# Kernel tuning notes

Hardware: AMD Instinct MI355X
Metric: run time of the kernel (lower is better)

Reference implementation:

```python
import jax, jax.numpy as jnp
import numpy as np

DIFF_Q = 0.8
ONE_OVER_DIFF_TOT = 0.05234482976098482

# roll shifts reproducing the 26 neighbor slices in make_pairs (periodic wrap).
# torch slice [2:] of the wrap-padded tensor == neighbor at +1 == jnp.roll(q, -1, axis)
SHIFTS = [
    (-1, 0, 0), (1, 0, 0), (0, -1, 0), (0, 1, 0), (0, 0, -1), (0, 0, 1),
    (-1, -1, 0), (1, -1, 0), (-1, 1, 0), (1, 1, 0),
    (-1, 0, -1), (1, 0, -1), (-1, 0, 1), (1, 0, 1),
    (0, -1, -1), (0, 1, -1), (0, -1, 1), (0, 1, 1),
    (-1, -1, -1), (-1, -1, 1), (-1, 1, -1), (-1, 1, 1),
    (1, -1, -1), (1, -1, 1), (1, 1, -1), (1, 1, 1),
]
# 6 face neighbors (d=1), 12 edge neighbors (d=sqrt2), 8 corner neighbors (d=sqrt3)
D_INV = jnp.asarray(np.array([1.0] * 6 + [2 ** -0.5] * 12 + [3 ** -0.5] * 8, dtype=np.float32))


def _mlp(x, params):
    # tanh-activated MLP, linear final layer (matches nn.Sequential built in __init__)
    for W, b in params[:-1]:
        x = jnp.tanh(x @ W.T + b)
    W, b = params[-1]
    return x @ W.T + b


def setup_inputs() -> dict:
    key = jax.random.key(0)
    ks = jax.random.split(key, 11)
    q = jax.random.uniform(ks[0], (1, 48, 48, 48, 2), dtype=jnp.float32)
    def lin(k, fan_out, fan_in):
        k1, k2 = jax.random.split(k)
        bound = 1.0 / np.sqrt(fan_in)
        W = jax.random.uniform(k1, (fan_out, fan_in), jnp.float32, -bound, bound)
        b = jax.random.uniform(k2, (fan_out,), jnp.float32, -bound, bound)
        return W, b
    W0, b0 = lin(ks[1], 16, 4)
    W1, b1 = lin(ks[2], 16, 16)
    W2, b2 = lin(ks[3], 16, 16)
    W3, b3 = lin(ks[4], 16, 16)
    Wout, bout = lin(ks[5], 1, 16)
    return {"q": q, "W0": W0, "b0": b0, "W1": W1, "b1": b1, "W2": W2, "b2": b2,
            "W3": W3, "b3": b3, "Wout": Wout, "bout": bout}


def reference(q, W0, b0, W1, b1, W2, b2, W3, b3, Wout, bout):
    # make_pairs detaches q, and q_updated starts from q.detach().clone()
    qd = jax.lax.stop_gradient(q)
    # neighbors: [B,X,Y,Z,26,2]
    nb = jnp.stack([jnp.roll(qd, s, axis=(1, 2, 3)) for s in SHIFTS], axis=4)
    own = jnp.broadcast_to(qd[:, :, :, :, None, :], nb.shape)
    x1 = jnp.concatenate([own, nb], axis=-1)  # [B,X,Y,Z,26,4]
    x2 = jnp.concatenate([nb, own], axis=-1)  # channel-rolled version
    params = [(W0, b0), (W1, b1), (W2, b2), (W3, b3), (Wout, bout)]
    transfer = jnp.tanh(_mlp(x1, params) - _mlp(x2, params))[..., 0]  # [B,X,Y,Z,26]
    # negative transfer scaled by own charge, positive by neighbor charge
    factor = jnp.where(transfer < 0, own[..., 0], nb[..., 0])
    transfer = (transfer * factor * D_INV).sum(axis=4) * (ONE_OVER_DIFF_TOT * DIFF_Q)
    return qd.at[..., 0].add(transfer)
```

## Files before the change

kernel.cpp:

```cpp
#include <hip/hip_runtime.h>

static constexpr int NSIDE = 48;
static constexpr int NVOX  = NSIDE * NSIDE * NSIDE;
static constexpr float SCALE = 0.041875863808787856f;
static constexpr int NDIR  = 13;
static constexpr int PAIRS_PER_BLOCK = 128;
static constexpr int BLOCKS_PER_DIR  = NVOX / PAIRS_PER_BLOCK;

typedef _Float16 f16x8 __attribute__((ext_vector_type(8)));
typedef float    f32x16 __attribute__((ext_vector_type(16)));

__device__ __constant__ int g_ox[NDIR] = { 1, 0, 0,  1, 1, 1, 1, 0, 0,  1, 1, 1, 1 };
__device__ __constant__ int g_oy[NDIR] = { 0, 1, 0,  1,-1, 0, 0, 1, 1,  1, 1,-1,-1 };
__device__ __constant__ int g_oz[NDIR] = { 0, 0, 1,  0, 0, 1,-1, 1,-1,  1,-1, 1,-1 };
__device__ __constant__ float g_dinv[NDIR] = {
    1.f, 1.f, 1.f,
    0.70710678118654752f, 0.70710678118654752f, 0.70710678118654752f,
    0.70710678118654752f, 0.70710678118654752f, 0.70710678118654752f,
    0.57735026918962576f, 0.57735026918962576f, 0.57735026918962576f, 0.57735026918962576f };

__device__ __constant__ int c_ox[26] = { 1,-1, 0, 0, 0, 0,
                                         1,-1, 1,-1, 1,-1, 1,-1, 0, 0, 0, 0,
                                         1, 1, 1, 1,-1,-1,-1,-1 };
__device__ __constant__ int c_oy[26] = { 0, 0, 1,-1, 0, 0,
                                         1, 1,-1,-1, 0, 0, 0, 0, 1,-1, 1,-1,
                                         1, 1,-1,-1, 1, 1,-1,-1 };
__device__ __constant__ int c_oz[26] = { 0, 0, 0, 0, 1,-1,
                                         0, 0, 0, 0, 1, 1,-1,-1, 1, 1,-1,-1,
                                         1,-1, 1,-1, 1,-1, 1,-1 };
__device__ __constant__ float c_dinv[26] = {
    1.f, 1.f, 1.f, 1.f, 1.f, 1.f,
    0.70710678118654752f, 0.70710678118654752f, 0.70710678118654752f, 0.70710678118654752f,
    0.70710678118654752f, 0.70710678118654752f, 0.70710678118654752f, 0.70710678118654752f,
    0.70710678118654752f, 0.70710678118654752f, 0.70710678118654752f, 0.70710678118654752f,
    0.57735026918962576f, 0.57735026918962576f, 0.57735026918962576f, 0.57735026918962576f,
    0.57735026918962576f, 0.57735026918962576f, 0.57735026918962576f, 0.57735026918962576f };

__device__ __forceinline__ float fast_tanh(float x) {
    float e = __builtin_amdgcn_exp2f(x * 2.8853900817779268f);
    float r = __builtin_amdgcn_rcpf(e + 1.0f);
    return fmaf(-2.0f, r, 1.0f);
}

#define STAGE_WEIGHTS()                                                        \
    __shared__ __align__(16) float sw[916];                                    \
    {                                                                          \
        const int t_ = threadIdx.x;                                            \
        if (t_ <  64) sw[      t_] = W0[t_];                                   \
        if (t_ <  16) sw[ 64 + t_] = b0[t_];                                   \
                      sw[ 80 + t_] = W1[t_];                                   \
        if (t_ <  16) sw[336 + t_] = b1[t_];                                   \
                      sw[352 + t_] = W2[t_];                                   \
        if (t_ <  16) sw[608 + t_] = b2[t_];                                   \
                      sw[624 + t_] = W3[t_];                                   \
        if (t_ <  16) sw[880 + t_] = b3[t_];                                   \
        if (t_ <  16) sw[896 + t_] = Wout[t_];                                 \
        if (t_ ==  0) sw[912]     = bout[0];                                   \
        __syncthreads();                                                       \
    }

#define SIG(G, P) (((P) < 4) ? 4 * (G) + (P) : 8 + 4 * (G) + ((P) - 4))

__global__ __launch_bounds__(256)
void flux_mfma_kernel(const float* __restrict__ q,
                      const float* __restrict__ W0, const float* __restrict__ b0,
                      const float* __restrict__ W1, const float* __restrict__ b1,
                      const float* __restrict__ W2, const float* __restrict__ b2,
                      const float* __restrict__ W3, const float* __restrict__ b3,
                      const float* __restrict__ Wout, const float* __restrict__ bout,
                      float* __restrict__ ws)
{
    STAGE_WEIGHTS()

    const int k    = blockIdx.x / BLOCKS_PER_DIR;
    const int rem  = blockIdx.x - k * BLOCKS_PER_DIR;
    const int lane = threadIdx.x & 63;
    const int wv   = threadIdx.x >> 6;
    const int g    = lane >> 5;
    const int vox  = rem * PAIRS_PER_BLOCK + wv * 32 + (lane & 31);

    const int z = vox % NSIDE;
    const int y = (vox / NSIDE) % NSIDE;
    const int x = vox / (NSIDE * NSIDE);
    const int ox = g_ox[k], oy = g_oy[k], oz = g_oz[k];
    const int nx = (ox > 0) ? ((x == NSIDE - 1) ? 0 : x + 1) : x;
    const int ny = (oy > 0) ? ((y == NSIDE - 1) ? 0 : y + 1)
                            : ((oy < 0) ? ((y == 0) ? NSIDE - 1 : y - 1) : y);
    const int nz = (oz > 0) ? ((z == NSIDE - 1) ? 0 : z + 1)
                            : ((oz < 0) ? ((z == 0) ? NSIDE - 1 : z - 1) : z);

    const float2 own = reinterpret_cast<const float2*>(q)[vox];
    const float2 nbq = reinterpret_cast<const float2*>(q)[(nx * NSIDE + ny) * NSIDE + nz];
    const float o0 = own.x, o1 = own.y;
    const float n0 = nbq.x, n1 = nbq.y;

    const int row = lane & 31;
    const int wr  = (row & 15) * 16;
    f16x8 aw1, aw2, aw3;
    f32x16 c1, c2, c3;
    #pragma unroll
    for (int p = 0; p < 8; ++p) {
        const int kk = SIG(g, p);
        aw1[p] = (_Float16)sw[ 80 + wr + kk];
        aw2[p] = (_Float16)sw[352 + wr + kk];
        aw3[p] = (_Float16)sw[624 + wr + kk];
        c1[p] = sw[336 + kk];
        c2[p] = sw[608 + kk];
        c3[p] = sw[880 + kk];
    }
    #pragma unroll
    for (int p = 8; p < 16; ++p) { c1[p] = 0.0f; c2[p] = 0.0f; c3[p] = 0.0f; }
    float woutv[8];
    #pragma unroll
    for (int p = 0; p < 8; ++p) woutv[p] = sw[896 + SIG(g, p)];

    f16x8 ba, bb;
    #pragma unroll
    for (int p = 0; p < 8; ++p) {
        const int f = SIG(g, p);
        const float4 w = *reinterpret_cast<const float4*>(&sw[f * 4]);
        const float bbias = sw[64 + f];
        float pa = fmaf(w.x, o0, fmaf(w.y, o1, fmaf(w.z, n0, fmaf(w.w, n1, bbias))));
        float pb = fmaf(w.x, n0, fmaf(w.y, n1, fmaf(w.z, o0, fmaf(w.w, o1, bbias))));
        ba[p] = (_Float16)fast_tanh(pa);
        bb[p] = (_Float16)fast_tanh(pb);
    }

    f32x16 da, db;
    da = __builtin_amdgcn_mfma_f32_32x32x16_f16(aw1, ba, c1, 0, 0, 0);
    db = __builtin_amdgcn_mfma_f32_32x32x16_f16(aw1, bb, c1, 0, 0, 0);
    #pragma unroll
    for (int p = 0; p < 8; ++p) {
        ba[p] = (_Float16)fast_tanh(da[p]);
        bb[p] = (_Float16)fast_tanh(db[p]);
    }
    da = __builtin_amdgcn_mfma_f32_32x32x16_f16(aw2, ba, c2, 0, 0, 0);
    db = __builtin_amdgcn_mfma_f32_32x32x16_f16(aw2, bb, c2, 0, 0, 0);
    #pragma unroll
    for (int p = 0; p < 8; ++p) {
        ba[p] = (_Float16)fast_tanh(da[p]);
        bb[p] = (_Float16)fast_tanh(db[p]);
    }
    da = __builtin_amdgcn_mfma_f32_32x32x16_f16(aw3, ba, c3, 0, 0, 0);
    db = __builtin_amdgcn_mfma_f32_32x32x16_f16(aw3, bb, c3, 0, 0, 0);

    float pa = 0.0f, pb = 0.0f;
    #pragma unroll
    for (int p = 0; p < 8; ++p) {
        pa = fmaf(fast_tanh(da[p]), woutv[p], pa);
        pb = fmaf(fast_tanh(db[p]), woutv[p], pb);
    }
    pa += __shfl_xor(pa, 32);
    pb += __shfl_xor(pb, 32);

    const float tr  = fast_tanh(pa - pb);
    const float fac = (tr < 0.0f) ? o0 : n0;
    if ((lane & 63) < 32)
        ws[k * NVOX + vox] = tr * fac * g_dinv[k];
}

__global__ __launch_bounds__(256)
void gather_kernel(const float* __restrict__ q,
                   const float* __restrict__ ws,
                   float* __restrict__ out)
{
    const int vox = blockIdx.x * 256 + threadIdx.x;

    const int z = vox % NSIDE;
    const int y = (vox / NSIDE) % NSIDE;
    const int x = vox / (NSIDE * NSIDE);
    const int xm = (x == 0) ? NSIDE - 1 : x - 1;
    const int ym = (y == 0) ? NSIDE - 1 : y - 1;
    const int yp = (y == NSIDE - 1) ? 0 : y + 1;
    const int zm = (z == 0) ? NSIDE - 1 : z - 1;
    const int zp = (z == NSIDE - 1) ? 0 : z + 1;

    float s = 0.0f;
    #pragma unroll
    for (int k = 0; k < NDIR; ++k) {
        const int px = g_ox[k] ? xm : x;
        const int py = (g_oy[k] > 0) ? ym : ((g_oy[k] < 0) ? yp : y);
        const int pz = (g_oz[k] > 0) ? zm : ((g_oz[k] < 0) ? zp : z);
        s += ws[k * NVOX + vox];
        s -= ws[k * NVOX + (px * NSIDE + py) * NSIDE + pz];
    }

    const float2 own = reinterpret_cast<const float2*>(q)[vox];
    float2 r;
    r.x = fmaf(s, SCALE, own.x);
    r.y = own.y;
    reinterpret_cast<float2*>(out)[vox] = r;
}

#define LAYER(WB, INA, INB, OUTA, OUTB)                                        \
    {                                                                          \
        _Pragma("unroll")                                                      \
        for (int i = 0; i < 16; ++i) {                                         \
            float aa = sw[(WB) + 256 + i];                                     \
            float ab = aa;                                                     \
            _Pragma("unroll")                                                  \
            for (int kk = 0; kk < 4; ++kk) {                                   \
                const float4 w = *reinterpret_cast<const float4*>(             \
                    &sw[(WB) + i * 16 + kk * 4]);                              \
                aa = fmaf(w.x, INA[4 * kk + 0], aa);                           \
                aa = fmaf(w.y, INA[4 * kk + 1], aa);                           \
                aa = fmaf(w.z, INA[4 * kk + 2], aa);                           \
                aa = fmaf(w.w, INA[4 * kk + 3], aa);                           \
                ab = fmaf(w.x, INB[4 * kk + 0], ab);                           \
                ab = fmaf(w.y, INB[4 * kk + 1], ab);                           \
                ab = fmaf(w.z, INB[4 * kk + 2], ab);                           \
                ab = fmaf(w.w, INB[4 * kk + 3], ab);                           \
            }                                                                  \
            OUTA[i] = fast_tanh(aa);                                           \
            OUTB[i] = fast_tanh(ab);                                           \
        }                                                                      \
    }

__global__ __launch_bounds__(256)
void automaton_kernel(const float* __restrict__ q,
                      const float* __restrict__ W0, const float* __restrict__ b0,
                      const float* __restrict__ W1, const float* __restrict__ b1,
                      const float* __restrict__ W2, const float* __restrict__ b2,
                      const float* __restrict__ W3, const float* __restrict__ b3,
                      const float* __restrict__ Wout, const float* __restrict__ bout,
                      float* __restrict__ out)
{
    STAGE_WEIGHTS()

    const int gid  = blockIdx.x * 256 + threadIdx.x;
    const int vox  = gid >> 1;
    const int half = gid & 1;

    const int z = vox % NSIDE;
    const int y = (vox / NSIDE) % NSIDE;
    const int x = vox / (NSIDE * NSIDE);
    const int xm = (x == 0) ? NSIDE - 1 : x - 1;
    const int xp = (x == NSIDE - 1) ? 0 : x + 1;
    const int ym = (y == 0) ? NSIDE - 1 : y - 1;
    const int yp = (y == NSIDE - 1) ? 0 : y + 1;
    const int zm = (z == 0) ? NSIDE - 1 : z - 1;
    const int zp = (z == NSIDE - 1) ? 0 : z + 1;

    const float2 own = reinterpret_cast<const float2*>(q)[vox];
    const float o0 = own.x, o1 = own.y;

    float sum = 0.0f;
    #pragma unroll 1
    for (int k = half * 13; k < half * 13 + 13; ++k) {
        asm volatile("" ::: "memory");
        const int ox = c_ox[k], oy = c_oy[k], oz = c_oz[k];
        const int nx = (ox < 0) ? xm : ((ox > 0) ? xp : x);
        const int ny = (oy < 0) ? ym : ((oy > 0) ? yp : y);
        const int nz = (oz < 0) ? zm : ((oz > 0) ? zp : z);
        const float2 nbq = reinterpret_cast<const float2*>(q)[(nx * NSIDE + ny) * NSIDE + nz];
        const float n0 = nbq.x, n1 = nbq.y;

        float ha[16], hb[16], ta[16], tb[16];
        #pragma unroll
        for (int i = 0; i < 16; ++i) {
            const float4 w = *reinterpret_cast<const float4*>(&sw[i * 4]);
            const float bbias = sw[64 + i];
            float pa = fmaf(w.x, o0, fmaf(w.y, o1, fmaf(w.z, n0, fmaf(w.w, n1, bbias))));
            float pb = fmaf(w.x, n0, fmaf(w.y, n1, fmaf(w.z, o0, fmaf(w.w, o1, bbias))));
            ha[i] = fast_tanh(pa);
            hb[i] = fast_tanh(pb);
        }
        LAYER(80,  ha, hb, ta, tb)
        LAYER(352, ta, tb, ha, hb)
        LAYER(624, ha, hb, ta, tb)
        float oa = sw[912], ob = sw[912];
        #pragma unroll
        for (int kk = 0; kk < 4; ++kk) {
            const float4 w = *reinterpret_cast<const float4*>(&sw[896 + kk * 4]);
            oa = fmaf(w.x, ta[4 * kk + 0], oa);
            oa = fmaf(w.y, ta[4 * kk + 1], oa);
            oa = fmaf(w.z, ta[4 * kk + 2], oa);
            oa = fmaf(w.w, ta[4 * kk + 3], oa);
            ob = fmaf(w.x, tb[4 * kk + 0], ob);
            ob = fmaf(w.y, tb[4 * kk + 1], ob);
            ob = fmaf(w.z, tb[4 * kk + 2], ob);
            ob = fmaf(w.w, tb[4 * kk + 3], ob);
        }
        const float tr  = fast_tanh(oa - ob);
        const float fac = (tr < 0.0f) ? o0 : n0;
        sum = fmaf(tr * fac, c_dinv[k], sum);
    }

    sum += __shfl_xor(sum, 1);
    if (half == 0) {
        float2 r;
        r.x = fmaf(sum, SCALE, o0);
        r.y = o1;
        reinterpret_cast<float2*>(out)[vox] = r;
    }
}

extern "C" void kernel_launch(void* const* d_in, const int* in_sizes, int n_in,
                              void* d_out, int out_size, void* d_ws, size_t ws_size,
                              hipStream_t stream) {
    const float* q    = (const float*)d_in[0];
    const float* W0   = (const float*)d_in[1];
    const float* b0   = (const float*)d_in[2];
    const float* W1   = (const float*)d_in[3];
    const float* b1   = (const float*)d_in[4];
    const float* W2   = (const float*)d_in[5];
    const float* b2   = (const float*)d_in[6];
    const float* W3   = (const float*)d_in[7];
    const float* b3   = (const float*)d_in[8];
    const float* Wout = (const float*)d_in[9];
    const float* bout = (const float*)d_in[10];
    float* out = (float*)d_out;

    const size_t ws_needed = (size_t)NDIR * NVOX * sizeof(float);
    if (ws_size >= ws_needed) {
        float* ws = (float*)d_ws;
        flux_mfma_kernel<<<dim3(NDIR * BLOCKS_PER_DIR), dim3(256), 0, stream>>>(
            q, W0, b0, W1, b1, W2, b2, W3, b3, Wout, bout, ws);
        gather_kernel<<<dim3(NVOX / 256), dim3(256), 0, stream>>>(q, ws, out);
    } else {
        automaton_kernel<<<dim3(NVOX * 2 / 256), dim3(256), 0, stream>>>(
            q, W0, b0, W1, b1, W2, b2, W3, b3, Wout, bout, out);
    }
}
```

Measured before the change: 63.80 us.

## Move first MLP layer onto MFMA and replace tanh with shared-reciprocal Pade

The first layer (4->16) now runs as an MFMA with zero-padded weights and inputs, instead of per-lane scalar FMAs. The hidden-layer tanh switches from exp2+rcp to a clamped [7/6] Pade rational approximation that shares one reciprocal between the two branch evaluations. This cuts transcendental instructions and scalar FMA work, at the cost of two extra MFMAs and reduced tanh accuracy for large inputs. The clamp keeps outputs in [-1,1], but the approximation error near saturation may matter for correctness tolerance.

```diff
diff --git a/kernel.cpp b/kernel.cpp
--- a/kernel.cpp
+++ b/kernel.cpp
@@ -42,6 +42,19 @@
     return fmaf(-2.0f, r, 1.0f);
 }
 
+__device__ __forceinline__ void pade_tanh_duo(float xa, float xb, float& ta, float& tb) {
+    const float ua = xa * xa, ub = xb * xb;
+    const float na = fmaf(ua, ua + 105.0f, 945.0f);
+    const float nb = fmaf(ub, ub + 105.0f, 945.0f);
+    const float ea = fmaf(ua, fmaf(ua, 15.0f, 420.0f), 945.0f);
+    const float eb = fmaf(ub, fmaf(ub, 15.0f, 420.0f), 945.0f);
+    const float R  = __builtin_amdgcn_rcpf(ea * eb);
+    ta = (xa * na) * (eb * R);
+    tb = (xb * nb) * (ea * R);
+    ta = fminf(1.0f, fmaxf(-1.0f, ta));
+    tb = fminf(1.0f, fmaxf(-1.0f, tb));
+}
+
 #define STAGE_WEIGHTS()                                                        \
     __shared__ __align__(16) float sw[916];                                    \
     {                                                                          \
@@ -95,51 +108,68 @@
     const float n0 = nbq.x, n1 = nbq.y;
 
     const int row = lane & 31;
-    const int wr  = (row & 15) * 16;
-    f16x8 aw1, aw2, aw3;
-    f32x16 c1, c2, c3;
+    f16x8 aw0, aw1, aw2, aw3;
+    f32x16 c0, c1, c2, c3;
     #pragma unroll
     for (int p = 0; p < 8; ++p) {
         const int kk = SIG(g, p);
-        aw1[p] = (_Float16)sw[ 80 + wr + kk];
-        aw2[p] = (_Float16)sw[352 + wr + kk];
-        aw3[p] = (_Float16)sw[624 + wr + kk];
+        aw0[p] = (row < 16 && kk < 4) ? (_Float16)sw[row * 4 + kk] : (_Float16)0.0f;
+        const float w1v = (row < 16) ? sw[ 80 + (row & 15) * 16 + kk] : 0.0f;
+        const float w2v = (row < 16) ? sw[352 + (row & 15) * 16 + kk] : 0.0f;
+        const float w3v = (row < 16) ? sw[624 + (row & 15) * 16 + kk] : 0.0f;
+        aw1[p] = (_Float16)w1v;
+        aw2[p] = (_Float16)w2v;
+        aw3[p] = (_Float16)w3v;
+        c0[p] = sw[ 64 + kk];
         c1[p] = sw[336 + kk];
         c2[p] = sw[608 + kk];
         c3[p] = sw[880 + kk];
     }
     #pragma unroll
-    for (int p = 8; p < 16; ++p) { c1[p] = 0.0f; c2[p] = 0.0f; c3[p] = 0.0f; }
+    for (int p = 8; p < 16; ++p) { c0[p] = 0.0f; c1[p] = 0.0f; c2[p] = 0.0f; c3[p] = 0.0f; }
     float woutv[8];
     #pragma unroll
     for (int p = 0; p < 8; ++p) woutv[p] = sw[896 + SIG(g, p)];
 
     f16x8 ba, bb;
-    #pragma unroll
-    for (int p = 0; p < 8; ++p) {
-        const int f = SIG(g, p);
-        const float4 w = *reinterpret_cast<const float4*>(&sw[f * 4]);
-        const float bbias = sw[64 + f];
-        float pa = fmaf(w.x, o0, fmaf(w.y, o1, fmaf(w.z, n0, fmaf(w.w, n1, bbias))));
-        float pb = fmaf(w.x, n0, fmaf(w.y, n1, fmaf(w.z, o0, fmaf(w.w, o1, bbias))));
-        ba[p] = (_Float16)fast_tanh(pa);
-        bb[p] = (_Float16)fast_tanh(pb);
+    {
+        const float va[4] = { o0, o1, n0, n1 };
+        #pragma unroll
+        for (int p = 0; p < 8; ++p) {
+            const float fa = (g == 0 && p < 4) ? va[p & 3]       : 0.0f;
+            const float fb = (g == 0 && p < 4) ? va[(p & 3) ^ 2] : 0.0f;
+            ba[p] = (_Float16)fa;
+            bb[p] = (_Float16)fb;
+        }
     }
 
     f32x16 da, db;
+    da = __builtin_amdgcn_mfma_f32_32x32x16_f16(aw0, ba, c0, 0, 0, 0);
+    db = __builtin_amdgcn_mfma_f32_32x32x16_f16(aw0, bb, c0, 0, 0, 0);
+    #pragma unroll
+    for (int p = 0; p < 8; ++p) {
+        float ta, tb;
+        pade_tanh_duo(da[p], db[p], ta, tb);
+        ba[p] = (_Float16)ta;
+        bb[p] = (_Float16)tb;
+    }
     da = __builtin_amdgcn_mfma_f32_32x32x16_f16(aw1, ba, c1, 0, 0, 0);
     db = __builtin_amdgcn_mfma_f32_32x32x16_f16(aw1, bb, c1, 0, 0, 0);
     #pragma unroll
     for (int p = 0; p < 8; ++p) {
-        ba[p] = (_Float16)fast_tanh(da[p]);
-        bb[p] = (_Float16)fast_tanh(db[p]);
+        float ta, tb;
+        pade_tanh_duo(da[p], db[p], ta, tb);
+        ba[p] = (_Float16)ta;
+        bb[p] = (_Float16)tb;
     }
     da = __builtin_amdgcn_mfma_f32_32x32x16_f16(aw2, ba, c2, 0, 0, 0);
     db = __builtin_amdgcn_mfma_f32_32x32x16_f16(aw2, bb, c2, 0, 0, 0);
     #pragma unroll
     for (int p = 0; p < 8; ++p) {
-        ba[p] = (_Float16)fast_tanh(da[p]);
-        bb[p] = (_Float16)fast_tanh(db[p]);
+        float ta, tb;
+        pade_tanh_duo(da[p], db[p], ta, tb);
+        ba[p] = (_Float16)ta;
+        bb[p] = (_Float16)tb;
     }
     da = __builtin_amdgcn_mfma_f32_32x32x16_f16(aw3, ba, c3, 0, 0, 0);
     db = __builtin_amdgcn_mfma_f32_32x32x16_f16(aw3, bb, c3, 0, 0, 0);
@@ -147,15 +177,17 @@
     float pa = 0.0f, pb = 0.0f;
     #pragma unroll
     for (int p = 0; p < 8; ++p) {
-        pa = fmaf(fast_tanh(da[p]), woutv[p], pa);
-        pb = fmaf(fast_tanh(db[p]), woutv[p], pb);
+        float ta, tb;
+        pade_tanh_duo(da[p], db[p], ta, tb);
+        pa = fmaf(ta, woutv[p], pa);
+        pb = fmaf(tb, woutv[p], pb);
     }
     pa += __shfl_xor(pa, 32);
     pb += __shfl_xor(pb, 32);
 
     const float tr  = fast_tanh(pa - pb);
     const float fac = (tr < 0.0f) ? o0 : n0;
-    if ((lane & 63) < 32)
+    if (lane < 32)
         ws[k * NVOX + vox] = tr * fac * g_dinv[k];
 }
 
```

After: 83.35 us. +30.6%, slower.

## Loop over several directions per flux block to amortize weight staging

Applied to the files above, without the earlier changes.

The flux kernel now launches one block per group of voxels and a slice, with each block iterating over 3-4 neighbor directions instead of handling a single direction. Weight staging into shared memory, MFMA weight-fragment setup, own-charge load and wrap index computation are done once per block and reused across directions. This reduces redundant setup work and block launch overhead, at the cost of fewer blocks and serial per-block work that may reduce latency hiding.

```diff
diff --git a/kernel.cpp b/kernel.cpp
--- a/kernel.cpp
+++ b/kernel.cpp
@@ -4,8 +4,9 @@
 static constexpr int NVOX  = NSIDE * NSIDE * NSIDE;
 static constexpr float SCALE = 0.041875863808787856f;
 static constexpr int NDIR  = 13;
-static constexpr int PAIRS_PER_BLOCK = 128;
-static constexpr int BLOCKS_PER_DIR  = NVOX / PAIRS_PER_BLOCK;
+static constexpr int NVOXGRP = NVOX / 32;
+static constexpr int NSLICE  = 4;
+static constexpr int FLUX_BLOCKS = NVOXGRP;
 
 typedef _Float16 f16x8 __attribute__((ext_vector_type(8)));
 typedef float    f32x16 __attribute__((ext_vector_type(16)));
@@ -42,7 +43,7 @@
     return fmaf(-2.0f, r, 1.0f);
 }
 
-#define STAGE_WEIGHTS()                                                        \
+#define STAGE_WEIGHTS_256()                                                    \
     __shared__ __align__(16) float sw[916];                                    \
     {                                                                          \
         const int t_ = threadIdx.x;                                            \
@@ -70,32 +71,28 @@
                       const float* __restrict__ Wout, const float* __restrict__ bout,
                       float* __restrict__ ws)
 {
-    STAGE_WEIGHTS()
-
-    const int k    = blockIdx.x / BLOCKS_PER_DIR;
-    const int rem  = blockIdx.x - k * BLOCKS_PER_DIR;
-    const int lane = threadIdx.x & 63;
-    const int wv   = threadIdx.x >> 6;
-    const int g    = lane >> 5;
-    const int vox  = rem * PAIRS_PER_BLOCK + wv * 32 + (lane & 31);
+    STAGE_WEIGHTS_256()
+
+    const int lane  = threadIdx.x & 63;
+    const int wv    = threadIdx.x >> 6;
+    const int g     = lane >> 5;
+    const int slice = blockIdx.x / (FLUX_BLOCKS / NSLICE);
+    const int vgrp  = (blockIdx.x % (FLUX_BLOCKS / NSLICE)) * 4 + wv;
+    const int vox   = vgrp * 32 + (lane & 31);
 
     const int z = vox % NSIDE;
     const int y = (vox / NSIDE) % NSIDE;
     const int x = vox / (NSIDE * NSIDE);
-    const int ox = g_ox[k], oy = g_oy[k], oz = g_oz[k];
-    const int nx = (ox > 0) ? ((x == NSIDE - 1) ? 0 : x + 1) : x;
-    const int ny = (oy > 0) ? ((y == NSIDE - 1) ? 0 : y + 1)
-                            : ((oy < 0) ? ((y == 0) ? NSIDE - 1 : y - 1) : y);
-    const int nz = (oz > 0) ? ((z == NSIDE - 1) ? 0 : z + 1)
-                            : ((oz < 0) ? ((z == 0) ? NSIDE - 1 : z - 1) : z);
+    const int xp = (x == NSIDE - 1) ? 0 : x + 1;
+    const int ym = (y == 0) ? NSIDE - 1 : y - 1;
+    const int yp = (y == NSIDE - 1) ? 0 : y + 1;
+    const int zm = (z == 0) ? NSIDE - 1 : z - 1;
+    const int zp = (z == NSIDE - 1) ? 0 : z + 1;
 
     const float2 own = reinterpret_cast<const float2*>(q)[vox];
-    const float2 nbq = reinterpret_cast<const float2*>(q)[(nx * NSIDE + ny) * NSIDE + nz];
     const float o0 = own.x, o1 = own.y;
-    const float n0 = nbq.x, n1 = nbq.y;
-
-    const int row = lane & 31;
-    const int wr  = (row & 15) * 16;
+
+    const int wr = (lane & 15) * 16;
     f16x8 aw1, aw2, aw3;
     f32x16 c1, c2, c3;
     #pragma unroll
@@ -114,49 +111,64 @@
     #pragma unroll
     for (int p = 0; p < 8; ++p) woutv[p] = sw[896 + SIG(g, p)];
 
-    f16x8 ba, bb;
-    #pragma unroll
-    for (int p = 0; p < 8; ++p) {
-        const int f = SIG(g, p);
-        const float4 w = *reinterpret_cast<const float4*>(&sw[f * 4]);
-        const float bbias = sw[64 + f];
-        float pa = fmaf(w.x, o0, fmaf(w.y, o1, fmaf(w.z, n0, fmaf(w.w, n1, bbias))));
-        float pb = fmaf(w.x, n0, fmaf(w.y, n1, fmaf(w.z, o0, fmaf(w.w, o1, bbias))));
-        ba[p] = (_Float16)fast_tanh(pa);
-        bb[p] = (_Float16)fast_tanh(pb);
-    }
-
-    f32x16 da, db;
-    da = __builtin_amdgcn_mfma_f32_32x32x16_f16(aw1, ba, c1, 0, 0, 0);
-    db = __builtin_amdgcn_mfma_f32_32x32x16_f16(aw1, bb, c1, 0, 0, 0);
-    #pragma unroll
-    for (int p = 0; p < 8; ++p) {
-        ba[p] = (_Float16)fast_tanh(da[p]);
-        bb[p] = (_Float16)fast_tanh(db[p]);
-    }
-    da = __builtin_amdgcn_mfma_f32_32x32x16_f16(aw2, ba, c2, 0, 0, 0);
-    db = __builtin_amdgcn_mfma_f32_32x32x16_f16(aw2, bb, c2, 0, 0, 0);
-    #pragma unroll
-    for (int p = 0; p < 8; ++p) {
-        ba[p] = (_Float16)fast_tanh(da[p]);
-        bb[p] = (_Float16)fast_tanh(db[p]);
-    }
-    da = __builtin_amdgcn_mfma_f32_32x32x16_f16(aw3, ba, c3, 0, 0, 0);
-    db = __builtin_amdgcn_mfma_f32_32x32x16_f16(aw3, bb, c3, 0, 0, 0);
-
-    float pa = 0.0f, pb = 0.0f;
-    #pragma unroll
-    for (int p = 0; p < 8; ++p) {
-        pa = fmaf(fast_tanh(da[p]), woutv[p], pa);
-        pb = fmaf(fast_tanh(db[p]), woutv[p], pb);
-    }
-    pa += __shfl_xor(pa, 32);
-    pb += __shfl_xor(pb, 32);
-
-    const float tr  = fast_tanh(pa - pb);
-    const float fac = (tr < 0.0f) ? o0 : n0;
-    if ((lane & 63) < 32)
-        ws[k * NVOX + vox] = tr * fac * g_dinv[k];
+    const int kb = (slice == 0) ? 0 : (slice == 1) ? 4 : (slice == 2) ? 7 : 10;
+    const int ke = (slice == 0) ? 4 : (slice == 1) ? 7 : (slice == 2) ? 10 : 13;
+
+    #pragma unroll 1
+    for (int k = kb; k < ke; ++k) {
+        asm volatile("" ::: "memory");
+
+        const int ox = g_ox[k], oy = g_oy[k], oz = g_oz[k];
+        const int nx = ox ? xp : x;
+        const int ny = (oy > 0) ? yp : ((oy < 0) ? ym : y);
+        const int nz = (oz > 0) ? zp : ((oz < 0) ? zm : z);
+        const float2 nbq = reinterpret_cast<const float2*>(q)[(nx * NSIDE + ny) * NSIDE + nz];
+        const float n0 = nbq.x, n1 = nbq.y;
+
+        f16x8 ba, bb;
+        #pragma unroll
+        for (int p = 0; p < 8; ++p) {
+            const int f = SIG(g, p);
+            const float4 w = *reinterpret_cast<const float4*>(&sw[f * 4]);
+            const float bbias = sw[64 + f];
+            float pa = fmaf(w.x, o0, fmaf(w.y, o1, fmaf(w.z, n0, fmaf(w.w, n1, bbias))));
+            float pb = fmaf(w.x, n0, fmaf(w.y, n1, fmaf(w.z, o0, fmaf(w.w, o1, bbias))));
+            ba[p] = (_Float16)fast_tanh(pa);
+            bb[p] = (_Float16)fast_tanh(pb);
+        }
+
+        f32x16 da, db;
+        da = __builtin_amdgcn_mfma_f32_32x32x16_f16(aw1, ba, c1, 0, 0, 0);
+        db = __builtin_amdgcn_mfma_f32_32x32x16_f16(aw1, bb, c1, 0, 0, 0);
+        #pragma unroll
+        for (int p = 0; p < 8; ++p) {
+            ba[p] = (_Float16)fast_tanh(da[p]);
+            bb[p] = (_Float16)fast_tanh(db[p]);
+        }
+        da = __builtin_amdgcn_mfma_f32_32x32x16_f16(aw2, ba, c2, 0, 0, 0);
+        db = __builtin_amdgcn_mfma_f32_32x32x16_f16(aw2, bb, c2, 0, 0, 0);
+        #pragma unroll
+        for (int p = 0; p < 8; ++p) {
+            ba[p] = (_Float16)fast_tanh(da[p]);
+            bb[p] = (_Float16)fast_tanh(db[p]);
+        }
+        da = __builtin_amdgcn_mfma_f32_32x32x16_f16(aw3, ba, c3, 0, 0, 0);
+        db = __builtin_amdgcn_mfma_f32_32x32x16_f16(aw3, bb, c3, 0, 0, 0);
+
+        float pa = 0.0f, pb = 0.0f;
+        #pragma unroll
+        for (int p = 0; p < 8; ++p) {
+            pa = fmaf(fast_tanh(da[p]), woutv[p], pa);
+            pb = fmaf(fast_tanh(db[p]), woutv[p], pb);
+        }
+        pa += __shfl_xor(pa, 32);
+        pb += __shfl_xor(pb, 32);
+
+        const float tr  = fast_tanh(pa - pb);
+        const float fac = (tr < 0.0f) ? o0 : n0;
+        if (lane < 32)
+            ws[k * NVOX + vox] = tr * fac * g_dinv[k];
+    }
 }
 
 __global__ __launch_bounds__(256)
@@ -225,7 +237,7 @@
                       const float* __restrict__ Wout, const float* __restrict__ bout,
                       float* __restrict__ out)
 {
-    STAGE_WEIGHTS()
+    STAGE_WEIGHTS_256()
 
     const int gid  = blockIdx.x * 256 + threadIdx.x;
     const int vox  = gid >> 1;
@@ -314,7 +326,7 @@
     const size_t ws_needed = (size_t)NDIR * NVOX * sizeof(float);
     if (ws_size >= ws_needed) {
         float* ws = (float*)d_ws;
-        flux_mfma_kernel<<<dim3(NDIR * BLOCKS_PER_DIR), dim3(256), 0, stream>>>(
+        flux_mfma_kernel<<<dim3(FLUX_BLOCKS), dim3(256), 0, stream>>>(
             q, W0, b0, W1, b1, W2, b2, W3, b3, Wout, bout, ws);
         gather_kernel<<<dim3(NVOX / 256), dim3(256), 0, stream>>>(q, ws, out);
     } else {
```

Measured after the change: 68.98 us. 1.08x slower.
